# Kernel optimization log

Hardware: AMD Instinct MI355X
Metric: run time of the kernel (lower is better)

## Reference

```python
import jax, jax.numpy as jnp
import numpy as np

NUM_HEADS = 4
HIDDEN = 128
LN_EPS = 1e-6
NEG_INF = -1e9


def setup_inputs() -> dict:
    key = jax.random.key(0)
    ks = jax.random.split(key, 8)
    B, S, H, NH = 64, 512, HIDDEN, NUM_HEADS
    enc = jax.random.normal(ks[0], (B, S, H), dtype=jnp.float32)
    mask = jax.random.randint(ks[1], (B, 1, S, S), 0, 2, dtype=jnp.int32)
    scale = 1.0 / np.sqrt(H)
    # torch Linear(H, H*NH, bias=False): weight is (H*NH, H); store transposed (H, H*NH)
    Wq = jax.random.normal(ks[2], (H, H * NH), dtype=jnp.float32) * scale
    Wk = jax.random.normal(ks[3], (H, H * NH), dtype=jnp.float32) * scale
    Wv = jax.random.normal(ks[4], (H, H * NH), dtype=jnp.float32) * scale
    Wo = jax.random.normal(ks[5], (H * NH, H), dtype=jnp.float32) * (1.0 / np.sqrt(H * NH))
    gamma = jnp.ones((H,), dtype=jnp.float32)
    beta = jnp.zeros((H,), dtype=jnp.float32)
    return {"enc": enc, "mask": mask, "Wq": Wq, "Wk": Wk, "Wv": Wv, "Wo": Wo, "gamma": gamma, "beta": beta}


def reference(enc, mask, Wq, Wk, Wv, Wo, gamma, beta):
    B, S, H = enc.shape
    NH = NUM_HEADS
    # projections -> (B, NH, S, H): each head has head_dim == hidden_units
    Q = (enc @ Wq).reshape(B, S, NH, H).transpose(0, 2, 1, 3)
    K = (enc @ Wk).reshape(B, S, NH, H).transpose(0, 2, 1, 3)
    V = (enc @ Wv).reshape(B, S, NH, H).transpose(0, 2, 1, 3)
    # scaled dot-product attention with mask (non-flash: full score matrix)
    scores = jnp.einsum('bhqd,bhkd->bhqk', Q, K) / jnp.sqrt(jnp.float32(H))
    scores = jnp.where(mask == 0, jnp.float32(NEG_INF), scores)
    attn = jax.nn.softmax(scores, axis=-1)  # dropout = identity in eval mode
    ctx = jnp.einsum('bhqk,bhkd->bhqd', attn, V)  # (B, NH, S, H)
    ctx = ctx.transpose(0, 2, 1, 3).reshape(B, S, NH * H)
    out = ctx @ Wo + enc  # dropout identity, residual add
    # LayerNorm over last dim
    mu = jnp.mean(out, axis=-1, keepdims=True)
    var = jnp.var(out, axis=-1, keepdims=True)
    return gamma * (out - mu) / jnp.sqrt(var + LN_EPS) + beta
```

## Files before the change

### kernel.cpp

```cpp
#include <hip/hip_runtime.h>
#include <stdint.h>

#define BATCH 64
#define SLEN 512
#define HID 128
#define NHEAD 4
#define DPROJ 512
#define MTOT (BATCH * SLEN)
#define SCALE 0.08838834764831845f
#define LOG2E 1.4426950408889634f

using short8 = __attribute__((ext_vector_type(8))) short;
using f32x4  = __attribute__((ext_vector_type(4))) float;
using u32x4  = __attribute__((ext_vector_type(4))) unsigned int;
using u32x2  = __attribute__((ext_vector_type(2))) unsigned int;
using us4    = __attribute__((ext_vector_type(4))) unsigned short;

__device__ __forceinline__ unsigned short f2bf(float f) {
  unsigned int u = __float_as_uint(f);
  u += 0x7fffu + ((u >> 16) & 1u);
  return (unsigned short)(u >> 16);
}

__global__ __launch_bounds__(256) void prep_kernel(
    const float* __restrict__ Wq,
    const float* __restrict__ Wk,
    const float* __restrict__ Wv,
    const float* __restrict__ Wo,
    const float* __restrict__ enc,
    const int* __restrict__ mask,
    unsigned short* __restrict__ WT,
    unsigned short* __restrict__ WoT,
    unsigned short* __restrict__ encb,
    unsigned int* __restrict__ mbits)
{
  if (blockIdx.x < 1024) {
    int idx = blockIdx.x * 256 + threadIdx.x;
    int z = idx >> 16;
    int i = idx & 65535;
    if (z < 3) {
      const float* W = (z == 0) ? Wq : (z == 1) ? Wk : Wv;
      float scale = (z == 0) ? (SCALE * LOG2E) : 1.0f;
      int k = i >> 9;
      int n = i & 511;
      WT[(size_t)z * 65536 + (size_t)n * 128 + k] = f2bf(W[i] * scale);
    } else {
      int k = i >> 7;
      int n = i & 127;
      WoT[(size_t)n * 512 + k] = f2bf(Wo[i]);
    }
  } else if (blockIdx.x < 3072) {
    size_t tid = (size_t)(blockIdx.x - 1024) * 256 + threadIdx.x;
    const float* s = enc + tid * 8;
    f32x4 a0 = *(const f32x4*)(s);
    f32x4 a1 = *(const f32x4*)(s + 4);
    short8 v;
    #pragma unroll
    for (int j = 0; j < 4; ++j) v[j] = (short)f2bf(a0[j]);
    #pragma unroll
    for (int j = 0; j < 4; ++j) v[4 + j] = (short)f2bf(a1[j]);
    *(short8*)(encb + tid * 8) = v;
  } else {
    const int l = threadIdx.x & 63;
    size_t wavebase = (size_t)(blockIdx.x - 3072) * 1024 + (threadIdx.x >> 6) * 256;
    unsigned long long b0 = __ballot(mask[wavebase + 0 * 64 + l] != 0);
    unsigned long long b1 = __ballot(mask[wavebase + 1 * 64 + l] != 0);
    unsigned long long b2 = __ballot(mask[wavebase + 2 * 64 + l] != 0);
    unsigned long long b3 = __ballot(mask[wavebase + 3 * 64 + l] != 0);
    if (l < 4) {
      unsigned long long v = (l & 2) ? ((l & 1) ? b3 : b2) : ((l & 1) ? b1 : b0);
      *(unsigned long long*)(mbits + (wavebase >> 5) + l * 2) = v;
    }
  }
}

__global__ __launch_bounds__(256) void qkv_kernel(
    const unsigned short* __restrict__ encb,
    const unsigned short* __restrict__ WT,
    unsigned short* __restrict__ Qh,
    unsigned short* __restrict__ Kh,
    unsigned short* __restrict__ Vt)
{
  const int nt = blockIdx.x;
  const int mt = blockIdx.y;
  const int t = threadIdx.x;
  const int lane = t & 63;
  const int w = t >> 6;
  const int quad = lane >> 4;
  const int l16 = lane & 15;

  __shared__ __align__(16) unsigned short Ald[128 * 136];
  __shared__ __align__(16) unsigned short Bld[128 * 72];

  const int m0 = mt * 128, n0 = nt * 128;
  const int wm = (w >> 1) * 64, wn = (w & 1) * 64;

  #pragma unroll
  for (int i = 0; i < 8; ++i) {
    int idx = i * 256 + t;
    int row = idx >> 4;
    int col = (idx & 15) << 3;
    *(u32x4*)(Ald + row * 136 + col) =
        *(const u32x4*)(encb + (size_t)(m0 + row) * HID + col);
  }

  for (int z = 0; z < 3; ++z) {
    const unsigned short* Wz = WT + (size_t)z * DPROJ * HID;

    f32x4 acc[4][4];
    #pragma unroll
    for (int mi = 0; mi < 4; ++mi)
      #pragma unroll
      for (int ni = 0; ni < 4; ++ni)
        acc[mi][ni] = f32x4{0.f, 0.f, 0.f, 0.f};

    #pragma unroll
    for (int kc = 0; kc < 2; ++kc) {
      __syncthreads();
      #pragma unroll
      for (int i = 0; i < 4; ++i) {
        int idx = i * 256 + t;
        int row = idx >> 3;
        int col = (idx & 7) << 3;
        *(u32x4*)(Bld + row * 72 + col) =
            *(const u32x4*)(Wz + (size_t)(n0 + row) * HID + kc * 64 + col);
      }
      __syncthreads();

      #pragma unroll
      for (int kk = 0; kk < 2; ++kk) {
        short8 a[4], bb[4];
        #pragma unroll
        for (int mi = 0; mi < 4; ++mi)
          a[mi] = *(const short8*)(Ald + (wm + mi * 16 + l16) * 136 + kc * 64 + kk * 32 + quad * 8);
        #pragma unroll
        for (int ni = 0; ni < 4; ++ni)
          bb[ni] = *(const short8*)(Bld + (wn + ni * 16 + l16) * 72 + kk * 32 + quad * 8);
        if (z < 2) {
          #pragma unroll
          for (int mi = 0; mi < 4; ++mi)
            #pragma unroll
            for (int ni = 0; ni < 4; ++ni)
              acc[mi][ni] = __builtin_amdgcn_mfma_f32_16x16x32_bf16(bb[ni], a[mi], acc[mi][ni], 0, 0, 0);
        } else {
          #pragma unroll
          for (int mi = 0; mi < 4; ++mi)
            #pragma unroll
            for (int ni = 0; ni < 4; ++ni)
              acc[mi][ni] = __builtin_amdgcn_mfma_f32_16x16x32_bf16(a[mi], bb[ni], acc[mi][ni], 0, 0, 0);
        }
      }
    }

    if (z < 2) {
      unsigned short* outz = ((z == 0) ? Qh : Kh) + (size_t)nt * MTOT * HID;
      #pragma unroll
      for (int mi = 0; mi < 4; ++mi)
        #pragma unroll
        for (int ni = 0; ni < 4; ++ni) {
          int m = m0 + wm + mi * 16 + l16;
          int dbase = wn + ni * 16 + quad * 4;
          us4 pk;
          #pragma unroll
          for (int r = 0; r < 4; ++r) pk[r] = f2bf(acc[mi][ni][r]);
          *(us4*)(outz + (size_t)m * HID + dbase) = pk;
        }
    } else {
      #pragma unroll
      for (int mi = 0; mi < 4; ++mi)
        #pragma unroll
        for (int ni = 0; ni < 4; ++ni) {
          int row0 = m0 + wm + mi * 16 + quad * 4;
          int b = row0 >> 9, s = row0 & 511;
          int d = wn + ni * 16 + l16;
          us4 pk;
          #pragma unroll
          for (int r = 0; r < 4; ++r) pk[r] = f2bf(acc[mi][ni][r]);
          *(us4*)(Vt + ((size_t)(nt * BATCH + b) * HID + d) * SLEN + s) = pk;
        }
    }
  }
}

__global__ __launch_bounds__(512, 4) void attn_kernel(
    const unsigned short* __restrict__ Qh,
    const unsigned short* __restrict__ Kh,
    const unsigned short* __restrict__ Vt,
    const unsigned int* __restrict__ mbits,
    unsigned short* __restrict__ ctx)
{
  const int lin = blockIdx.x;
  const int work = (lin & 7) * 128 + (lin >> 3);
  const int qt = work & 3;
  const int h  = (work >> 2) & 3;
  const int b  = work >> 4;

  const int t = threadIdx.x;
  const int lane = t & 63;
  const int w = t >> 6;
  const int quad = lane >> 4;
  const int l16 = lane & 15;

  __shared__ __align__(16) unsigned short Kld[64 * 136];
  __shared__ __align__(16) unsigned short Vtld[128 * 72];
  __shared__ __align__(16) unsigned short Pld[128 * 72];

  const int q0 = qt * 128;
  const size_t rowbase = (size_t)b * SLEN;
  const unsigned short* kbase0 = Kh + ((size_t)h * MTOT + rowbase) * HID;
  const unsigned short* vbase  = Vt + (size_t)(h * BATCH + b) * HID * SLEN;
  const unsigned int* mrow = mbits + (size_t)b * SLEN * 16;

  const int k_key = t >> 4, k_col = (t & 15) << 3;
  const int v_d   = t >> 3, v_cc  = (t & 7) << 3;

  short8 qa[4];
  {
    const unsigned short* qbase =
        Qh + ((size_t)h * MTOT + rowbase + q0 + w * 16 + l16) * HID + quad * 8;
    #pragma unroll
    for (int kk = 0; kk < 4; ++kk)
      qa[kk] = *(const short8*)(qbase + kk * 32);
  }

  short8 ones;
  #pragma unroll
  for (int j = 0; j < 8; ++j) ones[j] = (short)0x3F80;

  f32x4 oc[8], oc9;
  #pragma unroll
  for (int nd = 0; nd < 8; ++nd) oc[nd] = f32x4{0.f, 0.f, 0.f, 0.f};
  oc9 = f32x4{0.f, 0.f, 0.f, 0.f};

  u32x4 kreg[2], vreg[2];
  #pragma unroll
  for (int i = 0; i < 2; ++i) {
    kreg[i] = *(const u32x4*)(kbase0 + (size_t)(k_key + i * 32) * HID + k_col);
    vreg[i] = *(const u32x4*)(vbase + (size_t)(v_d + i * 64) * SLEN + v_cc);
  }

  for (int c0 = 0; c0 < SLEN; c0 += 64) {
    if (c0) __syncthreads();
    #pragma unroll
    for (int i = 0; i < 2; ++i) {
      *(u32x4*)(Kld + (k_key + i * 32) * 136 + k_col) = kreg[i];
      *(u32x4*)(Vtld + (v_d + i * 64) * 72 + v_cc) = vreg[i];
    }
    __syncthreads();
    if (c0 + 64 < SLEN) {
      #pragma unroll
      for (int i = 0; i < 2; ++i) {
        kreg[i] = *(const u32x4*)(kbase0 + (size_t)(c0 + 64 + k_key + i * 32) * HID + k_col);
        vreg[i] = *(const u32x4*)(vbase + (size_t)(v_d + i * 64) * SLEN + c0 + 64 + v_cc);
      }
    }

    u32x2 mw[4];
    #pragma unroll
    for (int r = 0; r < 4; ++r) {
      int qrow = q0 + w * 16 + quad * 4 + r;
      mw[r] = *(const u32x2*)(mrow + (size_t)qrow * 16 + (c0 >> 5));
    }

    f32x4 sc[4];
    #pragma unroll
    for (int ni = 0; ni < 4; ++ni) sc[ni] = f32x4{0.f, 0.f, 0.f, 0.f};
    #pragma unroll
    for (int kk = 0; kk < 4; ++kk) {
      #pragma unroll
      for (int ni = 0; ni < 4; ++ni) {
        short8 bb = *(const short8*)(Kld + (ni * 16 + l16) * 136 + kk * 32 + quad * 8);
        sc[ni] = __builtin_amdgcn_mfma_f32_16x16x32_bf16(qa[kk], bb, sc[ni], 0, 0, 0);
      }
    }

    #pragma unroll
    for (int ni = 0; ni < 4; ++ni) {
      int bit = (ni & 1) * 16 + l16;
      #pragma unroll
      for (int r = 0; r < 4; ++r) {
        unsigned wsel = (ni < 2) ? mw[r][0] : mw[r][1];
        float e = __builtin_amdgcn_exp2f(sc[ni][r]);
        float p = ((wsel >> bit) & 1u) ? e : 0.f;
        Pld[(w * 16 + quad * 4 + r) * 72 + ni * 16 + l16] = f2bf(p);
      }
    }
    __threadfence_block();

    #pragma unroll
    for (int kb = 0; kb < 2; ++kb) {
      short8 a = *(const short8*)(Pld + (w * 16 + l16) * 72 + kb * 32 + quad * 8);
      #pragma unroll
      for (int nd = 0; nd < 8; ++nd) {
        short8 bv = *(const short8*)(Vtld + (nd * 16 + l16) * 72 + kb * 32 + quad * 8);
        oc[nd] = __builtin_amdgcn_mfma_f32_16x16x32_bf16(a, bv, oc[nd], 0, 0, 0);
      }
      oc9 = __builtin_amdgcn_mfma_f32_16x16x32_bf16(a, ones, oc9, 0, 0, 0);
    }
  }

  float rcp[4];
  #pragma unroll
  for (int r = 0; r < 4; ++r) rcp[r] = __builtin_amdgcn_rcpf(oc9[r]);
  #pragma unroll
  for (int nd = 0; nd < 8; ++nd)
    #pragma unroll
    for (int r = 0; r < 4; ++r) {
      float val = oc[nd][r] * rcp[r];
      int row = q0 + w * 16 + quad * 4 + r;
      int col = h * HID + nd * 16 + l16;
      ctx[(rowbase + row) * DPROJ + col] = f2bf(val);
    }
}

__global__ __launch_bounds__(256, 4) void oproj_ln_kernel(
    const unsigned short* __restrict__ ctx,
    const unsigned short* __restrict__ WoT,
    const float* __restrict__ enc,
    const float* __restrict__ gamma,
    const float* __restrict__ beta,
    float* __restrict__ out)
{
  const int m0 = blockIdx.x * 64;
  const int t = threadIdx.x;
  const int lane = t & 63;
  const int w = t >> 6;
  const int quad = lane >> 4;
  const int l16 = lane & 15;

  __shared__ __align__(16) unsigned short Actx[64 * 72];
  __shared__ __align__(16) unsigned short Bw[128 * 72];

  f32x4 acc[8];
  #pragma unroll
  for (int ni = 0; ni < 8; ++ni) acc[ni] = f32x4{0.f, 0.f, 0.f, 0.f};

  for (int kc = 0; kc < DPROJ; kc += 64) {
    __syncthreads();
    #pragma unroll
    for (int i = 0; i < 2; ++i) {
      int idx = i * 256 + t;
      int row = idx >> 3;
      int col = (idx & 7) << 3;
      *(u32x4*)(Actx + row * 72 + col) =
          *(const u32x4*)(ctx + (size_t)(m0 + row) * DPROJ + kc + col);
    }
    #pragma unroll
    for (int i = 0; i < 4; ++i) {
      int idx = i * 256 + t;
      int row = idx >> 3;
      int col = (idx & 7) << 3;
      *(u32x4*)(Bw + row * 72 + col) =
          *(const u32x4*)(WoT + (size_t)row * DPROJ + kc + col);
    }
    __syncthreads();
    #pragma unroll
    for (int kk = 0; kk < 2; ++kk) {
      short8 a = *(const short8*)(Actx + (w * 16 + l16) * 72 + kk * 32 + quad * 8);
      #pragma unroll
      for (int ni = 0; ni < 8; ++ni) {
        short8 bb = *(const short8*)(Bw + (ni * 16 + l16) * 72 + kk * 32 + quad * 8);
        acc[ni] = __builtin_amdgcn_mfma_f32_16x16x32_bf16(a, bb, acc[ni], 0, 0, 0);
      }
    }
  }

  float g[8], be[8];
  #pragma unroll
  for (int ni = 0; ni < 8; ++ni) {
    g[ni] = gamma[ni * 16 + l16];
    be[ni] = beta[ni * 16 + l16];
  }

  float val[8][4];
  #pragma unroll
  for (int r = 0; r < 4; ++r) {
    int m = m0 + w * 16 + quad * 4 + r;
    const float* erow = enc + (size_t)m * HID;
    float s = 0.f, s2 = 0.f;
    #pragma unroll
    for (int ni = 0; ni < 8; ++ni) {
      float v = acc[ni][r] + erow[ni * 16 + l16];
      val[ni][r] = v;
      s += v;
      s2 += v * v;
    }
    #pragma unroll
    for (int off = 1; off < 16; off <<= 1) {
      s  += __shfl_xor(s, off, 64);
      s2 += __shfl_xor(s2, off, 64);
    }
    float mean = s * (1.f / 128.f);
    float var = s2 * (1.f / 128.f) - mean * mean;
    float rstd = rsqrtf(var + 1e-6f);
    float* orow = out + (size_t)m * HID;
    #pragma unroll
    for (int ni = 0; ni < 8; ++ni)
      orow[ni * 16 + l16] = g[ni] * (val[ni][r] - mean) * rstd + be[ni];
  }
}

extern "C" void kernel_launch(void* const* d_in, const int* in_sizes, int n_in,
                              void* d_out, int out_size, void* d_ws, size_t ws_size,
                              hipStream_t stream) {
  const float* enc   = (const float*)d_in[0];
  const int*   mask  = (const int*)d_in[1];
  const float* Wq    = (const float*)d_in[2];
  const float* Wk    = (const float*)d_in[3];
  const float* Wv    = (const float*)d_in[4];
  const float* Wo    = (const float*)d_in[5];
  const float* gamma = (const float*)d_in[6];
  const float* beta  = (const float*)d_in[7];
  float* out = (float*)d_out;

  unsigned short* WT  = (unsigned short*)d_ws;
  unsigned short* WoT = WT + (size_t)3 * DPROJ * HID;
  unsigned short* Qh  = WoT + (size_t)HID * DPROJ;
  unsigned short* Kh  = Qh + (size_t)NHEAD * MTOT * HID;
  unsigned short* Vt  = Kh + (size_t)NHEAD * MTOT * HID;
  unsigned short* ctx = Vt + (size_t)NHEAD * MTOT * HID;
  unsigned short* encb = ctx + (size_t)MTOT * DPROJ;
  unsigned int* mbits = (unsigned int*)(encb + (size_t)MTOT * HID * 2);

  prep_kernel<<<19456, 256, 0, stream>>>(Wq, Wk, Wv, Wo, enc, mask, WT, WoT, encb, mbits);
  qkv_kernel<<<dim3(4, 256), 256, 0, stream>>>(encb, WT, Qh, Kh, Vt);
  attn_kernel<<<1024, 512, 0, stream>>>(Qh, Kh, Vt, mbits, ctx);
  oproj_ln_kernel<<<MTOT / 64, 256, 0, stream>>>(ctx, WoT, enc, gamma, beta, out);
}
```

Before: 234.5 us.

## Give each attention wave two query row tiles to reuse K/V fragments

The attention kernel now runs 256 threads per block instead of 512, with each wave handling 32 query rows as two 16-row MFMA tiles. Each K and V fragment read from shared memory feeds two MFMAs, halving LDS traffic per unit of compute. The P tile in LDS uses an XOR swizzle to cut bank conflicts, and the V prefetch is moved after the score MFMAs to spread out global loads. In exchange each thread holds more accumulator registers (occupancy hint drops to 3) and loads twice as many K/V staging vectors.

```diff
diff --git a/kernel.cpp b/kernel.cpp
--- a/kernel.cpp
+++ b/kernel.cpp
@@ -182,7 +182,7 @@
   }
 }
 
-__global__ __launch_bounds__(512, 4) void attn_kernel(
+__global__ __launch_bounds__(256, 3) void attn_kernel(
     const unsigned short* __restrict__ Qh,
     const unsigned short* __restrict__ Kh,
     const unsigned short* __restrict__ Vt,
@@ -214,103 +214,125 @@
   const int k_key = t >> 4, k_col = (t & 15) << 3;
   const int v_d   = t >> 3, v_cc  = (t & 7) << 3;
 
-  short8 qa[4];
-  {
+  short8 qa[2][4];
+  #pragma unroll
+  for (int mi = 0; mi < 2; ++mi) {
     const unsigned short* qbase =
-        Qh + ((size_t)h * MTOT + rowbase + q0 + w * 16 + l16) * HID + quad * 8;
+        Qh + ((size_t)h * MTOT + rowbase + q0 + w * 32 + mi * 16 + l16) * HID + quad * 8;
     #pragma unroll
     for (int kk = 0; kk < 4; ++kk)
-      qa[kk] = *(const short8*)(qbase + kk * 32);
+      qa[mi][kk] = *(const short8*)(qbase + kk * 32);
   }
 
   short8 ones;
   #pragma unroll
   for (int j = 0; j < 8; ++j) ones[j] = (short)0x3F80;
 
-  f32x4 oc[8], oc9;
-  #pragma unroll
-  for (int nd = 0; nd < 8; ++nd) oc[nd] = f32x4{0.f, 0.f, 0.f, 0.f};
-  oc9 = f32x4{0.f, 0.f, 0.f, 0.f};
-
-  u32x4 kreg[2], vreg[2];
-  #pragma unroll
-  for (int i = 0; i < 2; ++i) {
-    kreg[i] = *(const u32x4*)(kbase0 + (size_t)(k_key + i * 32) * HID + k_col);
-    vreg[i] = *(const u32x4*)(vbase + (size_t)(v_d + i * 64) * SLEN + v_cc);
+  f32x4 oc[2][8], oc9[2];
+  #pragma unroll
+  for (int mi = 0; mi < 2; ++mi) {
+    #pragma unroll
+    for (int nd = 0; nd < 8; ++nd) oc[mi][nd] = f32x4{0.f, 0.f, 0.f, 0.f};
+    oc9[mi] = f32x4{0.f, 0.f, 0.f, 0.f};
+  }
+
+  u32x4 kreg[4], vreg[4];
+  #pragma unroll
+  for (int i = 0; i < 4; ++i) {
+    kreg[i] = *(const u32x4*)(kbase0 + (size_t)(k_key + i * 16) * HID + k_col);
+    vreg[i] = *(const u32x4*)(vbase + (size_t)(v_d + i * 32) * SLEN + v_cc);
   }
 
   for (int c0 = 0; c0 < SLEN; c0 += 64) {
     if (c0) __syncthreads();
     #pragma unroll
-    for (int i = 0; i < 2; ++i) {
-      *(u32x4*)(Kld + (k_key + i * 32) * 136 + k_col) = kreg[i];
-      *(u32x4*)(Vtld + (v_d + i * 64) * 72 + v_cc) = vreg[i];
+    for (int i = 0; i < 4; ++i) {
+      *(u32x4*)(Kld + (k_key + i * 16) * 136 + k_col) = kreg[i];
+      *(u32x4*)(Vtld + (v_d + i * 32) * 72 + v_cc) = vreg[i];
     }
     __syncthreads();
+
     if (c0 + 64 < SLEN) {
       #pragma unroll
-      for (int i = 0; i < 2; ++i) {
-        kreg[i] = *(const u32x4*)(kbase0 + (size_t)(c0 + 64 + k_key + i * 32) * HID + k_col);
-        vreg[i] = *(const u32x4*)(vbase + (size_t)(v_d + i * 64) * SLEN + c0 + 64 + v_cc);
-      }
-    }
-
-    u32x2 mw[4];
-    #pragma unroll
-    for (int r = 0; r < 4; ++r) {
-      int qrow = q0 + w * 16 + quad * 4 + r;
-      mw[r] = *(const u32x2*)(mrow + (size_t)qrow * 16 + (c0 >> 5));
-    }
-
-    f32x4 sc[4];
-    #pragma unroll
-    for (int ni = 0; ni < 4; ++ni) sc[ni] = f32x4{0.f, 0.f, 0.f, 0.f};
+      for (int i = 0; i < 4; ++i)
+        kreg[i] = *(const u32x4*)(kbase0 + (size_t)(c0 + 64 + k_key + i * 16) * HID + k_col);
+    }
+
+    f32x4 sc[2][4];
+    #pragma unroll
+    for (int mi = 0; mi < 2; ++mi)
+      #pragma unroll
+      for (int ni = 0; ni < 4; ++ni) sc[mi][ni] = f32x4{0.f, 0.f, 0.f, 0.f};
     #pragma unroll
     for (int kk = 0; kk < 4; ++kk) {
       #pragma unroll
       for (int ni = 0; ni < 4; ++ni) {
         short8 bb = *(const short8*)(Kld + (ni * 16 + l16) * 136 + kk * 32 + quad * 8);
-        sc[ni] = __builtin_amdgcn_mfma_f32_16x16x32_bf16(qa[kk], bb, sc[ni], 0, 0, 0);
-      }
-    }
-
-    #pragma unroll
-    for (int ni = 0; ni < 4; ++ni) {
-      int bit = (ni & 1) * 16 + l16;
+        sc[0][ni] = __builtin_amdgcn_mfma_f32_16x16x32_bf16(qa[0][kk], bb, sc[0][ni], 0, 0, 0);
+        sc[1][ni] = __builtin_amdgcn_mfma_f32_16x16x32_bf16(qa[1][kk], bb, sc[1][ni], 0, 0, 0);
+      }
+    }
+
+    if (c0 + 64 < SLEN) {
+      #pragma unroll
+      for (int i = 0; i < 4; ++i)
+        vreg[i] = *(const u32x4*)(vbase + (size_t)(v_d + i * 32) * SLEN + c0 + 64 + v_cc);
+    }
+
+    #pragma unroll
+    for (int mi = 0; mi < 2; ++mi) {
+      u32x2 mw[4];
       #pragma unroll
       for (int r = 0; r < 4; ++r) {
-        unsigned wsel = (ni < 2) ? mw[r][0] : mw[r][1];
-        float e = __builtin_amdgcn_exp2f(sc[ni][r]);
-        float p = ((wsel >> bit) & 1u) ? e : 0.f;
-        Pld[(w * 16 + quad * 4 + r) * 72 + ni * 16 + l16] = f2bf(p);
+        int qrow = q0 + w * 32 + mi * 16 + quad * 4 + r;
+        mw[r] = *(const u32x2*)(mrow + (size_t)qrow * 16 + (c0 >> 5));
+      }
+      #pragma unroll
+      for (int ni = 0; ni < 4; ++ni) {
+        int bit = (ni & 1) * 16 + l16;
+        int colsw = (ni * 16 + l16) ^ (quad << 3);
+        #pragma unroll
+        for (int r = 0; r < 4; ++r) {
+          unsigned wsel = (ni < 2) ? mw[r][0] : mw[r][1];
+          float e = __builtin_amdgcn_exp2f(sc[mi][ni][r]);
+          float p = ((wsel >> bit) & 1u) ? e : 0.f;
+          Pld[(w * 32 + mi * 16 + quad * 4 + r) * 72 + colsw] = f2bf(p);
+        }
       }
     }
     __threadfence_block();
 
+    const int rsw = (l16 >> 2) << 3;
     #pragma unroll
     for (int kb = 0; kb < 2; ++kb) {
-      short8 a = *(const short8*)(Pld + (w * 16 + l16) * 72 + kb * 32 + quad * 8);
+      short8 a0 = *(const short8*)(Pld + (w * 32 + l16) * 72 + ((kb * 32 + quad * 8) ^ rsw));
+      short8 a1 = *(const short8*)(Pld + (w * 32 + 16 + l16) * 72 + ((kb * 32 + quad * 8) ^ rsw));
       #pragma unroll
       for (int nd = 0; nd < 8; ++nd) {
         short8 bv = *(const short8*)(Vtld + (nd * 16 + l16) * 72 + kb * 32 + quad * 8);
-        oc[nd] = __builtin_amdgcn_mfma_f32_16x16x32_bf16(a, bv, oc[nd], 0, 0, 0);
-      }
-      oc9 = __builtin_amdgcn_mfma_f32_16x16x32_bf16(a, ones, oc9, 0, 0, 0);
-    }
-  }
-
-  float rcp[4];
-  #pragma unroll
-  for (int r = 0; r < 4; ++r) rcp[r] = __builtin_amdgcn_rcpf(oc9[r]);
-  #pragma unroll
-  for (int nd = 0; nd < 8; ++nd)
-    #pragma unroll
-    for (int r = 0; r < 4; ++r) {
-      float val = oc[nd][r] * rcp[r];
-      int row = q0 + w * 16 + quad * 4 + r;
-      int col = h * HID + nd * 16 + l16;
-      ctx[(rowbase + row) * DPROJ + col] = f2bf(val);
-    }
+        oc[0][nd] = __builtin_amdgcn_mfma_f32_16x16x32_bf16(a0, bv, oc[0][nd], 0, 0, 0);
+        oc[1][nd] = __builtin_amdgcn_mfma_f32_16x16x32_bf16(a1, bv, oc[1][nd], 0, 0, 0);
+      }
+      oc9[0] = __builtin_amdgcn_mfma_f32_16x16x32_bf16(a0, ones, oc9[0], 0, 0, 0);
+      oc9[1] = __builtin_amdgcn_mfma_f32_16x16x32_bf16(a1, ones, oc9[1], 0, 0, 0);
+    }
+  }
+
+  #pragma unroll
+  for (int mi = 0; mi < 2; ++mi) {
+    float rcp[4];
+    #pragma unroll
+    for (int r = 0; r < 4; ++r) rcp[r] = __builtin_amdgcn_rcpf(oc9[mi][r]);
+    #pragma unroll
+    for (int nd = 0; nd < 8; ++nd)
+      #pragma unroll
+      for (int r = 0; r < 4; ++r) {
+        float val = oc[mi][nd][r] * rcp[r];
+        int row = q0 + w * 32 + mi * 16 + quad * 4 + r;
+        int col = h * HID + nd * 16 + l16;
+        ctx[(rowbase + row) * DPROJ + col] = f2bf(val);
+      }
+  }
 }
 
 __global__ __launch_bounds__(256, 4) void oproj_ln_kernel(
@@ -424,6 +446,6 @@
 
   prep_kernel<<<19456, 256, 0, stream>>>(Wq, Wk, Wv, Wo, enc, mask, WT, WoT, encb, mbits);
   qkv_kernel<<<dim3(4, 256), 256, 0, stream>>>(encb, WT, Qh, Kh, Vt);
-  attn_kernel<<<1024, 512, 0, stream>>>(Qh, Kh, Vt, mbits, ctx);
+  attn_kernel<<<1024, 256, 0, stream>>>(Qh, Kh, Vt, mbits, ctx);
   oproj_ln_kernel<<<MTOT / 64, 256, 0, stream>>>(ctx, WoT, enc, gamma, beta, out);
 }
```

Measured after the change: 312.0 us. +33.1%, slower.

## Keep attention probabilities in registers via transposed MFMA and permlane swaps

Applied to the files above, without the earlier changes.

The score MFMA now uses swapped operands, so each lane holds a transposed score tile. The probabilities are packed to bf16 with v_cvt_pk_bf16_f32 and rearranged into the A-operand layout with permlane32/permlane16 swaps, which removes the Pld shared-memory round trip. The mask load drops to one 64-bit load per lane per chunk. The aim is less LDS traffic and shared memory use, at the cost of depending on exact lane permutation semantics and the new transposed mask bit indexing.

```diff
diff --git a/kernel.cpp b/kernel.cpp
--- a/kernel.cpp
+++ b/kernel.cpp
@@ -203,7 +203,6 @@
 
   __shared__ __align__(16) unsigned short Kld[64 * 136];
   __shared__ __align__(16) unsigned short Vtld[128 * 72];
-  __shared__ __align__(16) unsigned short Pld[128 * 72];
 
   const int q0 = qt * 128;
   const size_t rowbase = (size_t)b * SLEN;
@@ -239,6 +238,8 @@
     vreg[i] = *(const u32x4*)(vbase + (size_t)(v_d + i * 64) * SLEN + v_cc);
   }
 
+  const unsigned int* mq = mrow + (size_t)(q0 + w * 16 + l16) * 16;
+
   for (int c0 = 0; c0 < SLEN; c0 += 64) {
     if (c0) __syncthreads();
     #pragma unroll
@@ -255,12 +256,7 @@
       }
     }
 
-    u32x2 mw[4];
-    #pragma unroll
-    for (int r = 0; r < 4; ++r) {
-      int qrow = q0 + w * 16 + quad * 4 + r;
-      mw[r] = *(const u32x2*)(mrow + (size_t)qrow * 16 + (c0 >> 5));
-    }
+    u32x2 mw = *(const u32x2*)(mq + (c0 >> 5));
 
     f32x4 sc[4];
     #pragma unroll
@@ -270,26 +266,34 @@
       #pragma unroll
       for (int ni = 0; ni < 4; ++ni) {
         short8 bb = *(const short8*)(Kld + (ni * 16 + l16) * 136 + kk * 32 + quad * 8);
-        sc[ni] = __builtin_amdgcn_mfma_f32_16x16x32_bf16(qa[kk], bb, sc[ni], 0, 0, 0);
-      }
-    }
-
+        sc[ni] = __builtin_amdgcn_mfma_f32_16x16x32_bf16(bb, qa[kk], sc[ni], 0, 0, 0);
+      }
+    }
+
+    unsigned int pk[4][2];
     #pragma unroll
     for (int ni = 0; ni < 4; ++ni) {
-      int bit = (ni & 1) * 16 + l16;
+      unsigned wsel = (ni < 2) ? mw[0] : mw[1];
+      float p[4];
       #pragma unroll
       for (int r = 0; r < 4; ++r) {
-        unsigned wsel = (ni < 2) ? mw[r][0] : mw[r][1];
+        int bit = (ni & 1) * 16 + quad * 4 + r;
         float e = __builtin_amdgcn_exp2f(sc[ni][r]);
-        float p = ((wsel >> bit) & 1u) ? e : 0.f;
-        Pld[(w * 16 + quad * 4 + r) * 72 + ni * 16 + l16] = f2bf(p);
-      }
-    }
-    __threadfence_block();
+        p[r] = ((wsel >> bit) & 1u) ? e : 0.f;
+      }
+      asm("v_cvt_pk_bf16_f32 %0, %1, %2" : "=v"(pk[ni][0]) : "v"(p[0]), "v"(p[1]));
+      asm("v_cvt_pk_bf16_f32 %0, %1, %2" : "=v"(pk[ni][1]) : "v"(p[2]), "v"(p[3]));
+    }
 
     #pragma unroll
     for (int kb = 0; kb < 2; ++kb) {
-      short8 a = *(const short8*)(Pld + (w * 16 + l16) * 72 + kb * 32 + quad * 8);
+      unsigned int c0w = pk[kb * 2][0], c2w = pk[kb * 2 + 1][0];
+      asm("v_permlane32_swap_b32 %0, %1" : "+v"(c0w), "+v"(c2w));
+      asm("v_permlane16_swap_b32 %0, %1" : "+v"(c0w), "+v"(c2w));
+      unsigned int c1w = pk[kb * 2][1], c3w = pk[kb * 2 + 1][1];
+      asm("v_permlane32_swap_b32 %0, %1" : "+v"(c1w), "+v"(c3w));
+      asm("v_permlane16_swap_b32 %0, %1" : "+v"(c1w), "+v"(c3w));
+      short8 a = __builtin_bit_cast(short8, u32x4{c0w, c1w, c2w, c3w});
       #pragma unroll
       for (int nd = 0; nd < 8; ++nd) {
         short8 bv = *(const short8*)(Vtld + (nd * 16 + l16) * 72 + kb * 32 + quad * 8);
```

Result: faster. 228.7 us (-2.5%).
